# Optimization experiments

Measured on AMD Instinct MI355X. Metric: run time of the kernel, lower is better.

The kernel has to match this reference:

```python
import jax, jax.numpy as jnp
import numpy as np

N_VOX = 1_000_000
GRID = 192
C_IN, C_HID, C_OUT, KVOL = 3, 64, 3, 27
BN_EPS = 1e-5


def _build_neighbor_map(N=N_VOX, grid=GRID, seed=0):
    """Sample N unique voxel coords in a grid^3 volume and build the 27-offset
    kernel map (index of neighbor voxel per offset, -1 if absent), emulating
    MinkowskiEngine's coordinate-manager kernel map for stride-1 3x3x3 conv."""
    rng = np.random.default_rng(seed)
    keys = np.sort(rng.choice(grid ** 3, size=N, replace=False)).astype(np.int64)
    z = keys % grid
    y = (keys // grid) % grid
    x = keys // (grid * grid)
    offs = [(dx, dy, dz) for dx in (-1, 0, 1) for dy in (-1, 0, 1) for dz in (-1, 0, 1)]
    nbr = np.full((KVOL, N), -1, np.int32)
    for k, (dx, dy, dz) in enumerate(offs):
        nx, ny, nz = x + dx, y + dy, z + dz
        inb = (nx >= 0) & (nx < grid) & (ny >= 0) & (ny < grid) & (nz >= 0) & (nz < grid)
        nk = nx * grid * grid + ny * grid + nz
        pos = np.searchsorted(keys, nk).clip(0, N - 1)
        found = inb & (keys[pos] == nk)
        nbr[k] = np.where(found, pos, -1).astype(np.int32)
    return nbr


def setup_inputs() -> dict:
    key = jax.random.key(0)
    k1, k2, k3 = jax.random.split(key, 3)
    nbr = jnp.asarray(_build_neighbor_map())
    feats = jax.random.normal(k1, (N_VOX, C_IN), jnp.float32)
    W1 = jax.random.normal(k2, (KVOL, C_IN, C_HID), jnp.float32) * 0.1
    gamma = jnp.ones((C_HID,), jnp.float32)
    beta = jnp.zeros((C_HID,), jnp.float32)
    W2 = jax.random.normal(k3, (KVOL, C_HID, C_OUT), jnp.float32) * 0.05
    return {"feats": feats, "W1": W1, "gamma": gamma, "beta": beta,
            "W2": W2, "neighbor_idx": nbr}


def reference(feats, W1, gamma, beta, W2, neighbor_idx):
    N = feats.shape[0]
    mask = neighbor_idx >= 0                       # [27, N]
    idx = jnp.where(mask, neighbor_idx, 0)
    # --- sparse conv 3^3, stride 1: gather -> GEMM -> accumulate ---
    g = feats[idx] * mask[..., None]               # [27, N, 3]
    h = jnp.einsum('knc,kcd->nd', g, W1)           # [N, 64]
    # --- BatchNorm (training-mode batch stats) + ReLU ---
    mu = h.mean(0)
    var = h.var(0)
    h = (h - mu) * jax.lax.rsqrt(var + BN_EPS) * gamma + beta
    h = jax.nn.relu(h)
    # --- transposed conv, stride 1: same map with sign-flipped offsets ---
    idx_t = idx[::-1]
    mask_t = mask[::-1]
    def step(acc, kin):
        i, m, w = kin                               # i,m: [N], w: [64,3]
        return acc + jnp.where(m[:, None], h[i], 0.0) @ w, None
    out, _ = jax.lax.scan(step, jnp.zeros((N, C_OUT), feats.dtype),
                          (idx_t, mask_t, W2))
    return out
```

## Files before the change

### kernel.cpp

```cpp
#include <hip/hip_runtime.h>
#include <hip/hip_fp16.h>


#define KVOL 27
#define CHID 64

typedef _Float16 half2_t __attribute__((ext_vector_type(2)));
typedef unsigned int uint32;

static __device__ __forceinline__ float fdot2(uint32 u, uint32 w, float acc) {
    return __builtin_amdgcn_fdot2(__builtin_bit_cast(half2_t, u),
                                  __builtin_bit_cast(half2_t, w), acc, false);
}
static __device__ __forceinline__ uint32 pkh2(float a, float b) {
    auto p = __builtin_amdgcn_cvt_pkrtz(a, b);
    return __builtin_bit_cast(uint32, p);
}
static __device__ __forceinline__ uint32 pk_rne(float a, float b) {
    _Float16 ha = (_Float16)a, hb = (_Float16)b;
    unsigned short ua = __builtin_bit_cast(unsigned short, ha);
    unsigned short ub = __builtin_bit_cast(unsigned short, hb);
    return (uint32)ua | ((uint32)ub << 16);
}
static __device__ __forceinline__ void unpk(uint32 u, float& lo, float& hi) {
    half2_t h = __builtin_bit_cast(half2_t, u);
    lo = (float)h.x; hi = (float)h.y;
}

__global__ __launch_bounds__(256) void k_prep(
    const float* __restrict__ feats, const float* __restrict__ W1,
    const float* __restrict__ W2,
    float* __restrict__ f_t, float* __restrict__ W1t, uint32* __restrict__ w2q,
    uint32* __restrict__ h2, int N, int Ns)
{
    const int b = blockIdx.x;
    if (b == 0) {
        for (int i = threadIdx.x; i < 64 * 81; i += 256) {
            const int d = i / 81, kc = i % 81;
            W1t[i] = W1[kc * 64 + d];
        }
        for (int i = threadIdx.x; i < KVOL * 96; i += 256) {
            const int k = i / 96, r = i % 96;
            const int dc = r / 12, c = (r % 12) / 4, p = r & 3;
            const int d0 = dc * 8 + 2 * p;
            const float* src = W2 + (26 - k) * 192;
            w2q[i] = pk_rne(src[d0 * 3 + c], src[(d0 + 1) * 3 + c]);
        }
        for (int i = threadIdx.x; i < 3 * 64; i += 256) {
            const int c = i >> 6, pp = i & 63;
            f_t[(long long)c * Ns + N + pp] = 0.f;
        }
        for (int i = threadIdx.x; i < 8 * 4; i += 256) {
            const int dc = i >> 2, p = i & 3;
            h2[((long long)dc * Ns + N) * 4 + p] = 0u;
        }
    } else {
        __shared__ float tile[768];
        for (long long t0 = (long long)(b - 1) * 256; t0 < N;
             t0 += (long long)(gridDim.x - 1) * 256) {
            const int nrem = (int)min((long long)256, (long long)N - t0);
            __syncthreads();
            for (int i = threadIdx.x; i < 3 * nrem; i += 256)
                tile[i] = feats[t0 * 3 + i];
            __syncthreads();
            for (int i = threadIdx.x; i < nrem; i += 256) {
                f_t[0 * (long long)Ns + t0 + i] = tile[i * 3 + 0];
                f_t[1 * (long long)Ns + t0 + i] = tile[i * 3 + 1];
                f_t[2 * (long long)Ns + t0 + i] = tile[i * 3 + 2];
            }
        }
    }
}

__global__ __launch_bounds__(256) void k_conv1(
    const float* __restrict__ f_t, const float* __restrict__ W1t,
    const int* __restrict__ nbr, uint32* __restrict__ h2,
    int N, int Ns)
{
    const int lane = threadIdx.x & 63;
    const int tile = (int)((blockIdx.x * 256u + threadIdx.x) >> 6);
    const long long n0 = (long long)tile * 64;
    if (n0 >= N) return;
    const int n = (int)(n0 + lane);

    int j[KVOL];
#pragma unroll
    for (int k = 0; k < KVOL; ++k) j[k] = nbr[(long long)k * N + n];
#pragma unroll
    for (int k = 0; k < KVOL; ++k) j[k] = (j[k] < 0) ? N : j[k];

    float f[3 * KVOL];
#pragma unroll
    for (int k = 0; k < KVOL; ++k) {
        f[3 * k + 0] = f_t[j[k]];
        f[3 * k + 1] = f_t[Ns + j[k]];
        f[3 * k + 2] = f_t[2 * Ns + j[k]];
    }

#pragma unroll 2
    for (int t = 0; t < 32; ++t) {
        const float* __restrict__ w0 = W1t + (2 * t)     * 81;
        const float* __restrict__ w1 = W1t + (2 * t + 1) * 81;
        float a0 = 0.f, a1 = 0.f;
#pragma unroll
        for (int i = 0; i < 81; ++i) {
            a0 = fmaf(f[i], w0[i], a0);
            a1 = fmaf(f[i], w1[i], a1);
        }
        h2[((long long)(t >> 2) * Ns + n) * 4 + (t & 3)] = pkh2(a0, a1);
    }
}

__global__ __launch_bounds__(256) void k_stats(
    const uint32* __restrict__ h2, float* __restrict__ gstats, int N, int Ns)
{
    const int dc = blockIdx.y;
    const uint4* base = (const uint4*)(h2 + (long long)dc * Ns * 4);
    float s[8], q[8];
#pragma unroll
    for (int e = 0; e < 8; ++e) { s[e] = 0.f; q[e] = 0.f; }
    for (long long i = blockIdx.x * 256 + threadIdx.x; i < N;
         i += (long long)gridDim.x * 256) {
        const uint4 u = base[i];
        float lo, hi;
        unpk(u.x, lo, hi); s[0]+=lo; q[0]=fmaf(lo,lo,q[0]); s[1]+=hi; q[1]=fmaf(hi,hi,q[1]);
        unpk(u.y, lo, hi); s[2]+=lo; q[2]=fmaf(lo,lo,q[2]); s[3]+=hi; q[3]=fmaf(hi,hi,q[3]);
        unpk(u.z, lo, hi); s[4]+=lo; q[4]=fmaf(lo,lo,q[4]); s[5]+=hi; q[5]=fmaf(hi,hi,q[5]);
        unpk(u.w, lo, hi); s[6]+=lo; q[6]=fmaf(lo,lo,q[6]); s[7]+=hi; q[7]=fmaf(hi,hi,q[7]);
    }
#pragma unroll
    for (int e = 0; e < 8; ++e)
        for (int off = 32; off > 0; off >>= 1) {
            s[e] += __shfl_down(s[e], off);
            q[e] += __shfl_down(q[e], off);
        }
    __shared__ float red[4][16];
    const int wib = threadIdx.x >> 6, lane = threadIdx.x & 63;
    if (lane == 0) {
#pragma unroll
        for (int e = 0; e < 8; ++e) { red[wib][e] = s[e]; red[wib][8 + e] = q[e]; }
    }
    __syncthreads();
    if (threadIdx.x < 16) {
        const float v = red[0][threadIdx.x] + red[1][threadIdx.x]
                      + red[2][threadIdx.x] + red[3][threadIdx.x];
        const int e = threadIdx.x & 7;
        const int d = dc * 8 + e;
        atomicAdd(&gstats[threadIdx.x < 8 ? d : 64 + d], v);
    }
}

__global__ void k_bn(const float* __restrict__ gstats,
                     const float* __restrict__ gamma,
                     const float* __restrict__ beta,
                     float* __restrict__ sc_sh, float invN)
{
    const int d = threadIdx.x;
    const float mu  = gstats[d] * invN;
    const float var = gstats[64 + d] * invN - mu * mu;
    const float sc  = gamma[d] * rsqrtf(var + 1e-5f);
    sc_sh[d]      = sc;
    sc_sh[64 + d] = beta[d] - mu * sc;
}

__global__ __launch_bounds__(256) void k_apply(
    uint32* __restrict__ h2, const float* __restrict__ sc_sh, int N, int Ns)
{
    const int dc = blockIdx.y;
    float sc[8], sh[8];
#pragma unroll
    for (int e = 0; e < 8; ++e) {
        sc[e] = sc_sh[dc * 8 + e];
        sh[e] = sc_sh[64 + dc * 8 + e];
    }
    uint4* base = (uint4*)(h2 + (long long)dc * Ns * 4);
    for (long long i = blockIdx.x * 256 + threadIdx.x; i < N;
         i += (long long)gridDim.x * 256) {
        uint4 u = base[i];
        float lo, hi; uint4 r;
        unpk(u.x, lo, hi);
        r.x = pkh2(fmaxf(fmaf(lo, sc[0], sh[0]), 0.f), fmaxf(fmaf(hi, sc[1], sh[1]), 0.f));
        unpk(u.y, lo, hi);
        r.y = pkh2(fmaxf(fmaf(lo, sc[2], sh[2]), 0.f), fmaxf(fmaf(hi, sc[3], sh[3]), 0.f));
        unpk(u.z, lo, hi);
        r.z = pkh2(fmaxf(fmaf(lo, sc[4], sh[4]), 0.f), fmaxf(fmaf(hi, sc[5], sh[5]), 0.f));
        unpk(u.w, lo, hi);
        r.w = pkh2(fmaxf(fmaf(lo, sc[6], sh[6]), 0.f), fmaxf(fmaf(hi, sc[7], sh[7]), 0.f));
        base[i] = r;
    }
}

__global__ __launch_bounds__(256) void k_conv2(
    const uint32* __restrict__ h2, const uint32* __restrict__ w2q,
    const int* __restrict__ nbr, float* __restrict__ out,
    int N, int Ns, int nblk)
{
    const int bid = blockIdx.x;
    const int qq = nblk >> 3, rr = nblk & 7;
    const int xcd = bid & 7, pos = bid >> 3;
    const int sb = (xcd < rr) ? xcd * (qq + 1) + pos
                              : rr * (qq + 1) + (xcd - rr) * qq + pos;
    const int lane = threadIdx.x & 63;
    const int tile = sb * 4 + (threadIdx.x >> 6);
    const long long n0 = (long long)tile * 64;
    if (n0 >= N) return;
    const int n = (int)(n0 + lane);

    float a0 = 0.f, a1 = 0.f, a2 = 0.f;
    int jn = nbr[n];
    for (int k = 0; k < KVOL; ++k) {
        const int j = (jn < 0) ? N : jn;
        if (k + 1 < KVOL) jn = nbr[(long long)(k + 1) * N + n];

        uint4 u[8];
#pragma unroll
        for (int dc = 0; dc < 8; ++dc)
            u[dc] = *(const uint4*)(h2 + ((long long)dc * Ns + j) * 4);

        const uint32* __restrict__ w = w2q + k * 96;
#pragma unroll
        for (int dc = 0; dc < 8; ++dc) {
            const int wb = dc * 12;
            a0 = fdot2(u[dc].x, w[wb + 0], a0);
            a1 = fdot2(u[dc].x, w[wb + 4], a1);
            a2 = fdot2(u[dc].x, w[wb + 8], a2);
            a0 = fdot2(u[dc].y, w[wb + 1], a0);
            a1 = fdot2(u[dc].y, w[wb + 5], a1);
            a2 = fdot2(u[dc].y, w[wb + 9], a2);
            a0 = fdot2(u[dc].z, w[wb + 2], a0);
            a1 = fdot2(u[dc].z, w[wb + 6], a1);
            a2 = fdot2(u[dc].z, w[wb + 10], a2);
            a0 = fdot2(u[dc].w, w[wb + 3], a0);
            a1 = fdot2(u[dc].w, w[wb + 7], a1);
            a2 = fdot2(u[dc].w, w[wb + 11], a2);
        }
    }
    out[3LL * n + 0] = a0;
    out[3LL * n + 1] = a1;
    out[3LL * n + 2] = a2;
}

extern "C" void kernel_launch(void* const* d_in, const int* in_sizes, int n_in,
                              void* d_out, int out_size, void* d_ws, size_t ws_size,
                              hipStream_t stream) {
    const float* feats = (const float*)d_in[0];
    const float* W1    = (const float*)d_in[1];
    const float* gamma = (const float*)d_in[2];
    const float* beta  = (const float*)d_in[3];
    const float* W2    = (const float*)d_in[4];
    const int*   nbr   = (const int*)  d_in[5];
    const int N  = in_sizes[0] / 3;
    const int Ns = N + 64;
    float* out = (float*)d_out;

    char* ws = (char*)d_ws;
    uint32* h2 = (uint32*)ws;
    size_t off = (size_t)8 * Ns * 16;
    float* f_t = (float*)(ws + off);
    off += (size_t)3 * Ns * sizeof(float);
    float* W1t = (float*)(ws + off);
    off += (size_t)64 * 81 * sizeof(float);
    uint32* w2q = (uint32*)(ws + off);
    off += (size_t)KVOL * 96 * sizeof(uint32);
    float* gstats = (float*)(ws + off);
    float* sc_sh  = gstats + 128;

    (void)hipMemsetAsync(gstats, 0, 128 * sizeof(float), stream);

    const int ntiles = (N + 63) / 64;
    const int nblk   = (ntiles + 3) / 4;

    k_prep <<<257, 256, 0, stream>>>(feats, W1, W2, f_t, W1t, w2q, h2, N, Ns);
    k_conv1<<<nblk, 256, 0, stream>>>(f_t, W1t, nbr, h2, N, Ns);
    k_stats<<<dim3(256, 8), 256, 0, stream>>>(h2, gstats, N, Ns);
    k_bn   <<<1, 64, 0, stream>>>(gstats, gamma, beta, sc_sh, 1.0f / (float)N);
    k_apply<<<dim3(256, 8), 256, 0, stream>>>(h2, sc_sh, N, Ns);
    k_conv2<<<nblk, 256, 0, stream>>>(h2, w2q, nbr, out, N, Ns, nblk);
}
```

Before: 582.4 us.

## Compact valid neighbor pairs for conv2, fuse BN-ReLU into gather, fp16 conv1

A new pass compacts the valid (output, neighbor) pairs for each of the 27 offsets into a list. The second conv then walks only those pairs and accumulates into the output with atomics, so it no longer gathers h rows for absent neighbors. The BN scale and shift are applied as packed fp16 plus ReLU inside the conv2 gather, which removes the separate apply pass over h. Conv1 now packs features and weights to fp16 and uses dot2 instructions, and it counts valid neighbors per offset with ballots. In exchange there is an extra read of the neighbor map, pair-list writes, float atomics on the output with a memset, and more fp16 rounding.

```diff
diff --git a/kernel.cpp b/kernel.cpp
--- a/kernel.cpp
+++ b/kernel.cpp
@@ -7,6 +7,7 @@
 
 typedef _Float16 half2_t __attribute__((ext_vector_type(2)));
 typedef unsigned int uint32;
+typedef unsigned long long u64;
 
 static __device__ __forceinline__ float fdot2(uint32 u, uint32 w, float acc) {
     return __builtin_amdgcn_fdot2(__builtin_bit_cast(half2_t, u),
@@ -26,18 +27,37 @@
     half2_t h = __builtin_bit_cast(half2_t, u);
     lo = (float)h.x; hi = (float)h.y;
 }
+static __device__ __forceinline__ uint32 bnrelu(uint32 h, uint32 sc, uint32 sh) {
+    half2_t r = __builtin_bit_cast(half2_t, h) * __builtin_bit_cast(half2_t, sc)
+              + __builtin_bit_cast(half2_t, sh);
+    uint32 u = __builtin_bit_cast(uint32, r);
+    uint32 s = (u & 0x80008000u) >> 15;
+    return u & ~(s * 0xFFFFu);
+}
+
+#define M_GSTATS 0
+#define M_CNT8   128
+#define M_STARTS 344
+#define M_ENDS   372
+#define M_CURSOR 399
+#define M_SCPK   426
+#define M_SHPK   458
+#define M_WORDS  490
 
 __global__ __launch_bounds__(256) void k_prep(
     const float* __restrict__ feats, const float* __restrict__ W1,
     const float* __restrict__ W2,
-    float* __restrict__ f_t, float* __restrict__ W1t, uint32* __restrict__ w2q,
+    float* __restrict__ f_t, uint32* __restrict__ w1q, uint32* __restrict__ w2q,
     uint32* __restrict__ h2, int N, int Ns)
 {
     const int b = blockIdx.x;
     if (b == 0) {
-        for (int i = threadIdx.x; i < 64 * 81; i += 256) {
-            const int d = i / 81, kc = i % 81;
-            W1t[i] = W1[kc * 64 + d];
+        for (int i = threadIdx.x; i < 64 * 41; i += 256) {
+            const int d = i / 41, p = i % 41;
+            const int kc0 = 2 * p, kc1 = 2 * p + 1;
+            const float v0 = W1[kc0 * 64 + d];
+            const float v1 = (kc1 < 81) ? W1[kc1 * 64 + d] : 0.f;
+            w1q[i] = pk_rne(v0, v1);
         }
         for (int i = threadIdx.x; i < KVOL * 96; i += 256) {
             const int k = i / 96, r = i % 96;
@@ -72,43 +92,58 @@
     }
 }
 
-__global__ __launch_bounds__(256) void k_conv1(
-    const float* __restrict__ f_t, const float* __restrict__ W1t,
+__global__ __launch_bounds__(256, 4) void k_conv1(
+    const float* __restrict__ f_t, const uint32* __restrict__ w1q,
     const int* __restrict__ nbr, uint32* __restrict__ h2,
-    int N, int Ns)
-{
+    uint32* __restrict__ cnt8, int N, int Ns)
+{
+    __shared__ uint32 lcnt[KVOL];
+    if (threadIdx.x < KVOL) lcnt[threadIdx.x] = 0;
+    __syncthreads();
+
     const int lane = threadIdx.x & 63;
     const int tile = (int)((blockIdx.x * 256u + threadIdx.x) >> 6);
     const long long n0 = (long long)tile * 64;
-    if (n0 >= N) return;
-    const int n = (int)(n0 + lane);
-
-    int j[KVOL];
-#pragma unroll
-    for (int k = 0; k < KVOL; ++k) j[k] = nbr[(long long)k * N + n];
-#pragma unroll
-    for (int k = 0; k < KVOL; ++k) j[k] = (j[k] < 0) ? N : j[k];
-
-    float f[3 * KVOL];
-#pragma unroll
-    for (int k = 0; k < KVOL; ++k) {
-        f[3 * k + 0] = f_t[j[k]];
-        f[3 * k + 1] = f_t[Ns + j[k]];
-        f[3 * k + 2] = f_t[2 * Ns + j[k]];
-    }
+    const bool active = (n0 < N);
+
+    if (active) {
+        const int n = (int)(n0 + lane);
+        int j[KVOL];
+#pragma unroll
+        for (int k = 0; k < KVOL; ++k) {
+            const int jr = nbr[(long long)k * N + n];
+            const u64 m = __ballot(jr >= 0);
+            if (lane == 0) atomicAdd(&lcnt[k], (uint32)__popcll(m));
+            j[k] = (jr < 0) ? N : jr;
+        }
+
+        uint32 fh[41];
+#pragma unroll
+        for (int p = 0; p < 41; ++p) {
+            const int kc0 = 2 * p, kc1 = 2 * p + 1;
+            const float x0 = f_t[(long long)(kc0 % 3) * Ns + j[kc0 / 3]];
+            const float x1 = (kc1 < 81)
+                ? f_t[(long long)(kc1 % 3) * Ns + j[kc1 / 3]] : 0.f;
+            fh[p] = pkh2(x0, x1);
+        }
 
 #pragma unroll 2
-    for (int t = 0; t < 32; ++t) {
-        const float* __restrict__ w0 = W1t + (2 * t)     * 81;
-        const float* __restrict__ w1 = W1t + (2 * t + 1) * 81;
-        float a0 = 0.f, a1 = 0.f;
-#pragma unroll
-        for (int i = 0; i < 81; ++i) {
-            a0 = fmaf(f[i], w0[i], a0);
-            a1 = fmaf(f[i], w1[i], a1);
-        }
-        h2[((long long)(t >> 2) * Ns + n) * 4 + (t & 3)] = pkh2(a0, a1);
-    }
+        for (int t = 0; t < 32; ++t) {
+            const uint32* __restrict__ w0 = w1q + (2 * t) * 41;
+            const uint32* __restrict__ w1 = w1q + (2 * t + 1) * 41;
+            float a0 = 0.f, a1 = 0.f;
+#pragma unroll
+            for (int p = 0; p < 41; ++p) {
+                a0 = fdot2(fh[p], w0[p], a0);
+                a1 = fdot2(fh[p], w1[p], a1);
+            }
+            h2[((long long)(t >> 2) * Ns + n) * 4 + (t & 3)] = pkh2(a0, a1);
+        }
+    }
+
+    __syncthreads();
+    if (threadIdx.x < KVOL)
+        atomicAdd(&cnt8[(blockIdx.x & 7) * KVOL + threadIdx.x], lcnt[threadIdx.x]);
 }
 
 __global__ __launch_bounds__(256) void k_stats(
@@ -150,67 +185,114 @@
     }
 }
 
-__global__ void k_bn(const float* __restrict__ gstats,
-                     const float* __restrict__ gamma,
-                     const float* __restrict__ beta,
-                     float* __restrict__ sc_sh, float invN)
-{
-    const int d = threadIdx.x;
-    const float mu  = gstats[d] * invN;
-    const float var = gstats[64 + d] * invN - mu * mu;
-    const float sc  = gamma[d] * rsqrtf(var + 1e-5f);
-    sc_sh[d]      = sc;
-    sc_sh[64 + d] = beta[d] - mu * sc;
-}
-
-__global__ __launch_bounds__(256) void k_apply(
-    uint32* __restrict__ h2, const float* __restrict__ sc_sh, int N, int Ns)
-{
-    const int dc = blockIdx.y;
-    float sc[8], sh[8];
-#pragma unroll
-    for (int e = 0; e < 8; ++e) {
-        sc[e] = sc_sh[dc * 8 + e];
-        sh[e] = sc_sh[64 + dc * 8 + e];
-    }
-    uint4* base = (uint4*)(h2 + (long long)dc * Ns * 4);
-    for (long long i = blockIdx.x * 256 + threadIdx.x; i < N;
-         i += (long long)gridDim.x * 256) {
-        uint4 u = base[i];
-        float lo, hi; uint4 r;
-        unpk(u.x, lo, hi);
-        r.x = pkh2(fmaxf(fmaf(lo, sc[0], sh[0]), 0.f), fmaxf(fmaf(hi, sc[1], sh[1]), 0.f));
-        unpk(u.y, lo, hi);
-        r.y = pkh2(fmaxf(fmaf(lo, sc[2], sh[2]), 0.f), fmaxf(fmaf(hi, sc[3], sh[3]), 0.f));
-        unpk(u.z, lo, hi);
-        r.z = pkh2(fmaxf(fmaf(lo, sc[4], sh[4]), 0.f), fmaxf(fmaf(hi, sc[5], sh[5]), 0.f));
-        unpk(u.w, lo, hi);
-        r.w = pkh2(fmaxf(fmaf(lo, sc[6], sh[6]), 0.f), fmaxf(fmaf(hi, sc[7], sh[7]), 0.f));
-        base[i] = r;
+__global__ void k_scan(uint32* __restrict__ meta,
+                       const float* __restrict__ gamma,
+                       const float* __restrict__ beta, float invN)
+{
+    __shared__ float scv[64], shv[64];
+    __shared__ uint32 scnt[KVOL];
+    const int t = threadIdx.x;
+    if (t < KVOL) {
+        uint32 c = 0;
+        for (int r = 0; r < 8; ++r) c += meta[M_CNT8 + r * KVOL + t];
+        scnt[t] = c;
+    }
+    {
+        const float* gstats = (const float*)meta;
+        const float mu  = gstats[t] * invN;
+        const float var = gstats[64 + t] * invN - mu * mu;
+        const float sc  = gamma[t] * rsqrtf(var + 1e-5f);
+        scv[t] = sc;
+        shv[t] = beta[t] - mu * sc;
+    }
+    __syncthreads();
+    if (t == 0) {
+        uint32 s = 0;
+        for (int k = 0; k < KVOL; ++k) {
+            meta[M_STARTS + k] = s;
+            meta[M_CURSOR + k] = s;
+            meta[M_ENDS + k]   = s + scnt[k];
+            s += (scnt[k] + 63u) & ~63u;
+        }
+        meta[M_STARTS + KVOL] = s;
+    }
+    if (t < 32) {
+        meta[M_SCPK + t] = pk_rne(scv[2 * t], scv[2 * t + 1]);
+        meta[M_SHPK + t] = pk_rne(shv[2 * t], shv[2 * t + 1]);
+    }
+}
+
+__global__ __launch_bounds__(256) void k_fill(
+    const int* __restrict__ nbr, uint32* __restrict__ meta,
+    int2* __restrict__ pairs, int N, uint32 cap)
+{
+    __shared__ int lbuf[2048];
+    __shared__ uint32 wcnt[4];
+    __shared__ uint32 sbase, srun;
+    const int k = blockIdx.y;
+    const int nb = blockIdx.x * 2048;
+    const int tid = threadIdx.x;
+    const int wib = tid >> 6, lane = tid & 63;
+
+    uint32 mycnt = 0;
+#pragma unroll
+    for (int r = 0; r < 8; ++r) {
+        const int i = nb + r * 256 + tid;
+        const int v = (i < N) ? nbr[(long long)k * N + i] : -1;
+        lbuf[r * 256 + tid] = v;
+        mycnt += (v >= 0);
+    }
+    for (int off = 32; off > 0; off >>= 1) mycnt += __shfl_down(mycnt, off);
+    if (lane == 0) wcnt[wib] = mycnt;
+    __syncthreads();
+    if (tid == 0) {
+        const uint32 C = wcnt[0] + wcnt[1] + wcnt[2] + wcnt[3];
+        sbase = atomicAdd(&meta[M_CURSOR + k], C);
+        srun = 0;
+    }
+    __syncthreads();
+    const uint32 base = sbase;
+
+    for (int r = 0; r < 8; ++r) {
+        const int i = r * 256 + tid;
+        const int jv = lbuf[i];
+        const bool v = (jv >= 0);
+        const u64 m = __ballot(v);
+        if (lane == 0) wcnt[wib] = (uint32)__popcll(m);
+        __syncthreads();
+        uint32 woff = srun;
+        for (int w = 0; w < 4; ++w) if (w < wib) woff += wcnt[w];
+        const uint32 pos = woff + (uint32)__popcll(m & ((1ull << lane) - 1ull));
+        if (v && base + pos < cap)
+            pairs[base + pos] = make_int2(nb + i, jv);
+        __syncthreads();
+        if (tid == 0) srun += wcnt[0] + wcnt[1] + wcnt[2] + wcnt[3];
+        __syncthreads();
     }
 }
 
 __global__ __launch_bounds__(256) void k_conv2(
     const uint32* __restrict__ h2, const uint32* __restrict__ w2q,
-    const int* __restrict__ nbr, float* __restrict__ out,
-    int N, int Ns, int nblk)
-{
-    const int bid = blockIdx.x;
-    const int qq = nblk >> 3, rr = nblk & 7;
-    const int xcd = bid & 7, pos = bid >> 3;
-    const int sb = (xcd < rr) ? xcd * (qq + 1) + pos
-                              : rr * (qq + 1) + (xcd - rr) * qq + pos;
+    const uint32* __restrict__ meta, const int2* __restrict__ pairs,
+    float* __restrict__ out, int N, int Ns)
+{
     const int lane = threadIdx.x & 63;
-    const int tile = sb * 4 + (threadIdx.x >> 6);
-    const long long n0 = (long long)tile * 64;
-    if (n0 >= N) return;
-    const int n = (int)(n0 + lane);
-
-    float a0 = 0.f, a1 = 0.f, a2 = 0.f;
-    int jn = nbr[n];
-    for (int k = 0; k < KVOL; ++k) {
-        const int j = (jn < 0) ? N : jn;
-        if (k + 1 < KVOL) jn = nbr[(long long)(k + 1) * N + n];
+    const int wid = (blockIdx.x << 2) + (threadIdx.x >> 6);
+    const int nwv = gridDim.x << 2;
+    const uint32 P = meta[M_STARTS + KVOL];
+
+    uint32 scl[32], shl[32];
+#pragma unroll
+    for (int i = 0; i < 32; ++i) { scl[i] = meta[M_SCPK + i]; shl[i] = meta[M_SHPK + i]; }
+
+    for (uint32 base = (uint32)wid * 64u; base < P; base += (uint32)nwv * 64u) {
+        int k = 0;
+        while (k < KVOL - 1 && base >= meta[M_STARTS + k + 1]) ++k;
+        const uint32 send = meta[M_ENDS + k];
+        const uint32 idx = base + lane;
+        const bool act = idx < send;
+        int n = 0, j = N;
+        if (act) { const int2 pr = pairs[idx]; n = pr.x; j = pr.y; }
 
         uint4 u[8];
 #pragma unroll
@@ -218,26 +300,33 @@
             u[dc] = *(const uint4*)(h2 + ((long long)dc * Ns + j) * 4);
 
         const uint32* __restrict__ w = w2q + k * 96;
+        float a0 = 0.f, a1 = 0.f, a2 = 0.f;
 #pragma unroll
         for (int dc = 0; dc < 8; ++dc) {
-            const int wb = dc * 12;
-            a0 = fdot2(u[dc].x, w[wb + 0], a0);
-            a1 = fdot2(u[dc].x, w[wb + 4], a1);
-            a2 = fdot2(u[dc].x, w[wb + 8], a2);
-            a0 = fdot2(u[dc].y, w[wb + 1], a0);
-            a1 = fdot2(u[dc].y, w[wb + 5], a1);
-            a2 = fdot2(u[dc].y, w[wb + 9], a2);
-            a0 = fdot2(u[dc].z, w[wb + 2], a0);
-            a1 = fdot2(u[dc].z, w[wb + 6], a1);
-            a2 = fdot2(u[dc].z, w[wb + 10], a2);
-            a0 = fdot2(u[dc].w, w[wb + 3], a0);
-            a1 = fdot2(u[dc].w, w[wb + 7], a1);
-            a2 = fdot2(u[dc].w, w[wb + 11], a2);
-        }
-    }
-    out[3LL * n + 0] = a0;
-    out[3LL * n + 1] = a1;
-    out[3LL * n + 2] = a2;
+            const int wb = dc * 12, sb = dc * 4;
+            const uint32 h0 = bnrelu(u[dc].x, scl[sb + 0], shl[sb + 0]);
+            const uint32 h1 = bnrelu(u[dc].y, scl[sb + 1], shl[sb + 1]);
+            const uint32 h2w = bnrelu(u[dc].z, scl[sb + 2], shl[sb + 2]);
+            const uint32 h3 = bnrelu(u[dc].w, scl[sb + 3], shl[sb + 3]);
+            a0 = fdot2(h0, w[wb + 0], a0);
+            a1 = fdot2(h0, w[wb + 4], a1);
+            a2 = fdot2(h0, w[wb + 8], a2);
+            a0 = fdot2(h1, w[wb + 1], a0);
+            a1 = fdot2(h1, w[wb + 5], a1);
+            a2 = fdot2(h1, w[wb + 9], a2);
+            a0 = fdot2(h2w, w[wb + 2], a0);
+            a1 = fdot2(h2w, w[wb + 6], a1);
+            a2 = fdot2(h2w, w[wb + 10], a2);
+            a0 = fdot2(h3, w[wb + 3], a0);
+            a1 = fdot2(h3, w[wb + 7], a1);
+            a2 = fdot2(h3, w[wb + 11], a2);
+        }
+        if (act) {
+            atomicAdd(&out[3LL * n + 0], a0);
+            atomicAdd(&out[3LL * n + 1], a1);
+            atomicAdd(&out[3LL * n + 2], a2);
+        }
+    }
 }
 
 extern "C" void kernel_launch(void* const* d_in, const int* in_sizes, int n_in,
@@ -256,24 +345,21 @@
     char* ws = (char*)d_ws;
     uint32* h2 = (uint32*)ws;
     size_t off = (size_t)8 * Ns * 16;
-    float* f_t = (float*)(ws + off);
-    off += (size_t)3 * Ns * sizeof(float);
-    float* W1t = (float*)(ws + off);
-    off += (size_t)64 * 81 * sizeof(float);
-    uint32* w2q = (uint32*)(ws + off);
-    off += (size_t)KVOL * 96 * sizeof(uint32);
-    float* gstats = (float*)(ws + off);
-    float* sc_sh  = gstats + 128;
-
-    (void)hipMemsetAsync(gstats, 0, 128 * sizeof(float), stream);
-
-    const int ntiles = (N + 63) / 64;
-    const int nblk   = (ntiles + 3) / 4;
-
-    k_prep <<<257, 256, 0, stream>>>(feats, W1, W2, f_t, W1t, w2q, h2, N, Ns);
-    k_conv1<<<nblk, 256, 0, stream>>>(f_t, W1t, nbr, h2, N, Ns);
-    k_stats<<<dim3(256, 8), 256, 0, stream>>>(h2, gstats, N, Ns);
-    k_bn   <<<1, 64, 0, stream>>>(gstats, gamma, beta, sc_sh, 1.0f / (float)N);
-    k_apply<<<dim3(256, 8), 256, 0, stream>>>(h2, sc_sh, N, Ns);
-    k_conv2<<<nblk, 256, 0, stream>>>(h2, w2q, nbr, out, N, Ns, nblk);
-}
+    uint32* w2q = (uint32*)(ws + off); off += KVOL * 96 * 4;
+    uint32* meta = (uint32*)(ws + off); off += ((M_WORDS * 4 + 255) & ~255ull);
+    float*  f_t = (float*)(ws + off);
+    uint32* w1q = (uint32*)(ws + off + (size_t)3 * Ns * 4);
+    int2*   pairs = (int2*)(ws + off);
+    const uint32 cap = (uint32)((ws_size - off) / sizeof(int2));
+
+    (void)hipMemsetAsync(meta, 0, (M_CNT8 + 8 * KVOL) * 4, stream);
+    (void)hipMemsetAsync(out, 0, (size_t)out_size * 4, stream);
+
+    const int nblk = (N / 64 + 3) / 4;
+    k_prep <<<257, 256, 0, stream>>>(feats, W1, W2, f_t, w1q, w2q, h2, N, Ns);
+    k_conv1<<<nblk, 256, 0, stream>>>(f_t, w1q, nbr, h2, (uint32*)(meta + M_CNT8), N, Ns);
+    k_stats<<<dim3(256, 8), 256, 0, stream>>>(h2, (float*)meta, N, Ns);
+    k_scan <<<1, 64, 0, stream>>>(meta, gamma, beta, 1.0f / (float)N);
+    k_fill <<<dim3((N + 2047) / 2048, KVOL), 256, 0, stream>>>(nbr, meta, pairs, N, cap);
+    k_conv2<<<2048, 256, 0, stream>>>(h2, w2q, meta, pairs, out, N, Ns);
+}
```

Result: slower. 1.011 ms (+73.6%).

## Store hidden activations row-major per voxel and use fp16 dot2 in conv1

Applied to the files above, without the earlier changes.

The hidden fp16 tensor moves from eight channel-group planes to one contiguous 128-byte row per voxel. Each neighbour gather in conv2 now reads a single cache-line-sized row instead of eight 16-byte pieces spread across separate planes. Conv1 now packs gathered features and W1 into half2 and accumulates with fdot2, which halves the arithmetic instruction count at some cost in precision. Stats and apply are adapted to the interleaved layout, and occupancy hints are added to both conv kernels. The block count now assumes N is a multiple of 64.

```diff
diff --git a/kernel.cpp b/kernel.cpp
--- a/kernel.cpp
+++ b/kernel.cpp
@@ -3,7 +3,6 @@
 
 
 #define KVOL 27
-#define CHID 64
 
 typedef _Float16 half2_t __attribute__((ext_vector_type(2)));
 typedef unsigned int uint32;
@@ -30,19 +29,22 @@
 __global__ __launch_bounds__(256) void k_prep(
     const float* __restrict__ feats, const float* __restrict__ W1,
     const float* __restrict__ W2,
-    float* __restrict__ f_t, float* __restrict__ W1t, uint32* __restrict__ w2q,
-    uint32* __restrict__ h2, int N, int Ns)
+    float* __restrict__ f_t, uint32* __restrict__ w1q, uint32* __restrict__ w2q,
+    uint32* __restrict__ h32, int N, int Ns)
 {
     const int b = blockIdx.x;
     if (b == 0) {
-        for (int i = threadIdx.x; i < 64 * 81; i += 256) {
-            const int d = i / 81, kc = i % 81;
-            W1t[i] = W1[kc * 64 + d];
+        for (int i = threadIdx.x; i < 64 * 41; i += 256) {
+            const int d = i / 41, p = i % 41;
+            const int kc0 = 2 * p, kc1 = 2 * p + 1;
+            const float v0 = W1[kc0 * 64 + d];
+            const float v1 = (kc1 < 81) ? W1[kc1 * 64 + d] : 0.f;
+            w1q[i] = pk_rne(v0, v1);
         }
         for (int i = threadIdx.x; i < KVOL * 96; i += 256) {
             const int k = i / 96, r = i % 96;
-            const int dc = r / 12, c = (r % 12) / 4, p = r & 3;
-            const int d0 = dc * 8 + 2 * p;
+            const int g = r / 12, c = (r % 12) / 4, p = r & 3;
+            const int d0 = g * 8 + 2 * p;
             const float* src = W2 + (26 - k) * 192;
             w2q[i] = pk_rne(src[d0 * 3 + c], src[(d0 + 1) * 3 + c]);
         }
@@ -50,10 +52,8 @@
             const int c = i >> 6, pp = i & 63;
             f_t[(long long)c * Ns + N + pp] = 0.f;
         }
-        for (int i = threadIdx.x; i < 8 * 4; i += 256) {
-            const int dc = i >> 2, p = i & 3;
-            h2[((long long)dc * Ns + N) * 4 + p] = 0u;
-        }
+        if (threadIdx.x < 32)
+            h32[(long long)N * 32 + threadIdx.x] = 0u;
     } else {
         __shared__ float tile[768];
         for (long long t0 = (long long)(b - 1) * 256; t0 < N;
@@ -72,9 +72,9 @@
     }
 }
 
-__global__ __launch_bounds__(256) void k_conv1(
-    const float* __restrict__ f_t, const float* __restrict__ W1t,
-    const int* __restrict__ nbr, uint32* __restrict__ h2,
+__global__ __launch_bounds__(256, 4) void k_conv1(
+    const float* __restrict__ f_t, const uint32* __restrict__ w1q,
+    const int* __restrict__ nbr, uint32* __restrict__ h32,
     int N, int Ns)
 {
     const int lane = threadIdx.x & 63;
@@ -89,39 +89,48 @@
 #pragma unroll
     for (int k = 0; k < KVOL; ++k) j[k] = (j[k] < 0) ? N : j[k];
 
-    float f[3 * KVOL];
-#pragma unroll
-    for (int k = 0; k < KVOL; ++k) {
-        f[3 * k + 0] = f_t[j[k]];
-        f[3 * k + 1] = f_t[Ns + j[k]];
-        f[3 * k + 2] = f_t[2 * Ns + j[k]];
-    }
-
-#pragma unroll 2
-    for (int t = 0; t < 32; ++t) {
-        const float* __restrict__ w0 = W1t + (2 * t)     * 81;
-        const float* __restrict__ w1 = W1t + (2 * t + 1) * 81;
-        float a0 = 0.f, a1 = 0.f;
-#pragma unroll
-        for (int i = 0; i < 81; ++i) {
-            a0 = fmaf(f[i], w0[i], a0);
-            a1 = fmaf(f[i], w1[i], a1);
-        }
-        h2[((long long)(t >> 2) * Ns + n) * 4 + (t & 3)] = pkh2(a0, a1);
+    uint32 fh[41];
+#pragma unroll
+    for (int p = 0; p < 41; ++p) {
+        const int kc0 = 2 * p, kc1 = 2 * p + 1;
+        const float x0 = f_t[(long long)(kc0 % 3) * Ns + j[kc0 / 3]];
+        const float x1 = (kc1 < 81)
+            ? f_t[(long long)(kc1 % 3) * Ns + j[kc1 / 3]] : 0.f;
+        fh[p] = pkh2(x0, x1);
+    }
+
+    uint32* __restrict__ hrow = h32 + (long long)n * 32;
+#pragma unroll
+    for (int g = 0; g < 8; ++g) {
+        uint32 wd[4];
+#pragma unroll
+        for (int p4 = 0; p4 < 4; ++p4) {
+            const int t = 4 * g + p4;
+            const uint32* __restrict__ w0 = w1q + (2 * t) * 41;
+            const uint32* __restrict__ w1 = w1q + (2 * t + 1) * 41;
+            float a0 = 0.f, a1 = 0.f;
+#pragma unroll
+            for (int p = 0; p < 41; ++p) {
+                a0 = fdot2(fh[p], w0[p], a0);
+                a1 = fdot2(fh[p], w1[p], a1);
+            }
+            wd[p4] = pkh2(a0, a1);
+        }
+        *(uint4*)(hrow + 4 * g) = make_uint4(wd[0], wd[1], wd[2], wd[3]);
     }
 }
 
 __global__ __launch_bounds__(256) void k_stats(
-    const uint32* __restrict__ h2, float* __restrict__ gstats, int N, int Ns)
-{
-    const int dc = blockIdx.y;
-    const uint4* base = (const uint4*)(h2 + (long long)dc * Ns * 4);
+    const uint4* __restrict__ h4, float* __restrict__ gstats, int N)
+{
+    const int tid = threadIdx.x;
+    const int g = tid & 7;
     float s[8], q[8];
 #pragma unroll
     for (int e = 0; e < 8; ++e) { s[e] = 0.f; q[e] = 0.f; }
-    for (long long i = blockIdx.x * 256 + threadIdx.x; i < N;
-         i += (long long)gridDim.x * 256) {
-        const uint4 u = base[i];
+    const int total = N * 8;
+    for (int i = blockIdx.x * 256 + tid; i < total; i += gridDim.x * 256) {
+        const uint4 u = h4[i];
         float lo, hi;
         unpk(u.x, lo, hi); s[0]+=lo; q[0]=fmaf(lo,lo,q[0]); s[1]+=hi; q[1]=fmaf(hi,hi,q[1]);
         unpk(u.y, lo, hi); s[2]+=lo; q[2]=fmaf(lo,lo,q[2]); s[3]+=hi; q[3]=fmaf(hi,hi,q[3]);
@@ -129,24 +138,27 @@
         unpk(u.w, lo, hi); s[6]+=lo; q[6]=fmaf(lo,lo,q[6]); s[7]+=hi; q[7]=fmaf(hi,hi,q[7]);
     }
 #pragma unroll
-    for (int e = 0; e < 8; ++e)
-        for (int off = 32; off > 0; off >>= 1) {
-            s[e] += __shfl_down(s[e], off);
-            q[e] += __shfl_down(q[e], off);
-        }
-    __shared__ float red[4][16];
-    const int wib = threadIdx.x >> 6, lane = threadIdx.x & 63;
-    if (lane == 0) {
-#pragma unroll
-        for (int e = 0; e < 8; ++e) { red[wib][e] = s[e]; red[wib][8 + e] = q[e]; }
+    for (int e = 0; e < 8; ++e) {
+        for (int m = 8; m < 64; m <<= 1) {
+            s[e] += __shfl_xor(s[e], m);
+            q[e] += __shfl_xor(q[e], m);
+        }
+    }
+    __shared__ float sred[4][8][8], qred[4][8][8];
+    const int wib = tid >> 6, lane = tid & 63;
+    if (lane < 8) {
+#pragma unroll
+        for (int e = 0; e < 8; ++e) { sred[wib][lane][e] = s[e]; qred[wib][lane][e] = q[e]; }
     }
     __syncthreads();
-    if (threadIdx.x < 16) {
-        const float v = red[0][threadIdx.x] + red[1][threadIdx.x]
-                      + red[2][threadIdx.x] + red[3][threadIdx.x];
-        const int e = threadIdx.x & 7;
-        const int d = dc * 8 + e;
-        atomicAdd(&gstats[threadIdx.x < 8 ? d : 64 + d], v);
+    if (tid < 64) {
+        const int gg = tid >> 3, e = tid & 7;
+        atomicAdd(&gstats[tid], sred[0][gg][e] + sred[1][gg][e]
+                              + sred[2][gg][e] + sred[3][gg][e]);
+    } else if (tid < 128) {
+        const int d = tid - 64, gg = d >> 3, e = d & 7;
+        atomicAdd(&gstats[64 + d], qred[0][gg][e] + qred[1][gg][e]
+                                 + qred[2][gg][e] + qred[3][gg][e]);
     }
 }
 
@@ -164,19 +176,19 @@
 }
 
 __global__ __launch_bounds__(256) void k_apply(
-    uint32* __restrict__ h2, const float* __restrict__ sc_sh, int N, int Ns)
-{
-    const int dc = blockIdx.y;
+    uint4* __restrict__ h4, const float* __restrict__ sc_sh, int N)
+{
+    const int tid = threadIdx.x;
+    const int g = tid & 7;
     float sc[8], sh[8];
 #pragma unroll
     for (int e = 0; e < 8; ++e) {
-        sc[e] = sc_sh[dc * 8 + e];
-        sh[e] = sc_sh[64 + dc * 8 + e];
-    }
-    uint4* base = (uint4*)(h2 + (long long)dc * Ns * 4);
-    for (long long i = blockIdx.x * 256 + threadIdx.x; i < N;
-         i += (long long)gridDim.x * 256) {
-        uint4 u = base[i];
+        sc[e] = sc_sh[8 * g + e];
+        sh[e] = sc_sh[64 + 8 * g + e];
+    }
+    const int total = N * 8;
+    for (int i = blockIdx.x * 256 + tid; i < total; i += gridDim.x * 256) {
+        uint4 u = h4[i];
         float lo, hi; uint4 r;
         unpk(u.x, lo, hi);
         r.x = pkh2(fmaxf(fmaf(lo, sc[0], sh[0]), 0.f), fmaxf(fmaf(hi, sc[1], sh[1]), 0.f));
@@ -186,14 +198,14 @@
         r.z = pkh2(fmaxf(fmaf(lo, sc[4], sh[4]), 0.f), fmaxf(fmaf(hi, sc[5], sh[5]), 0.f));
         unpk(u.w, lo, hi);
         r.w = pkh2(fmaxf(fmaf(lo, sc[6], sh[6]), 0.f), fmaxf(fmaf(hi, sc[7], sh[7]), 0.f));
-        base[i] = r;
-    }
-}
-
-__global__ __launch_bounds__(256) void k_conv2(
-    const uint32* __restrict__ h2, const uint32* __restrict__ w2q,
+        h4[i] = r;
+    }
+}
+
+__global__ __launch_bounds__(256, 6) void k_conv2(
+    const uint4* __restrict__ h4, const uint32* __restrict__ w2q,
     const int* __restrict__ nbr, float* __restrict__ out,
-    int N, int Ns, int nblk)
+    int N, int nblk)
 {
     const int bid = blockIdx.x;
     const int qq = nblk >> 3, rr = nblk & 7;
@@ -212,27 +224,27 @@
         const int j = (jn < 0) ? N : jn;
         if (k + 1 < KVOL) jn = nbr[(long long)(k + 1) * N + n];
 
+        const uint4* __restrict__ row = h4 + (long long)j * 8;
         uint4 u[8];
 #pragma unroll
-        for (int dc = 0; dc < 8; ++dc)
-            u[dc] = *(const uint4*)(h2 + ((long long)dc * Ns + j) * 4);
+        for (int g = 0; g < 8; ++g) u[g] = row[g];
 
         const uint32* __restrict__ w = w2q + k * 96;
 #pragma unroll
-        for (int dc = 0; dc < 8; ++dc) {
-            const int wb = dc * 12;
-            a0 = fdot2(u[dc].x, w[wb + 0], a0);
-            a1 = fdot2(u[dc].x, w[wb + 4], a1);
-            a2 = fdot2(u[dc].x, w[wb + 8], a2);
-            a0 = fdot2(u[dc].y, w[wb + 1], a0);
-            a1 = fdot2(u[dc].y, w[wb + 5], a1);
-            a2 = fdot2(u[dc].y, w[wb + 9], a2);
-            a0 = fdot2(u[dc].z, w[wb + 2], a0);
-            a1 = fdot2(u[dc].z, w[wb + 6], a1);
-            a2 = fdot2(u[dc].z, w[wb + 10], a2);
-            a0 = fdot2(u[dc].w, w[wb + 3], a0);
-            a1 = fdot2(u[dc].w, w[wb + 7], a1);
-            a2 = fdot2(u[dc].w, w[wb + 11], a2);
+        for (int g = 0; g < 8; ++g) {
+            const int wb = g * 12;
+            a0 = fdot2(u[g].x, w[wb + 0], a0);
+            a1 = fdot2(u[g].x, w[wb + 4], a1);
+            a2 = fdot2(u[g].x, w[wb + 8], a2);
+            a0 = fdot2(u[g].y, w[wb + 1], a0);
+            a1 = fdot2(u[g].y, w[wb + 5], a1);
+            a2 = fdot2(u[g].y, w[wb + 9], a2);
+            a0 = fdot2(u[g].z, w[wb + 2], a0);
+            a1 = fdot2(u[g].z, w[wb + 6], a1);
+            a2 = fdot2(u[g].z, w[wb + 10], a2);
+            a0 = fdot2(u[g].w, w[wb + 3], a0);
+            a1 = fdot2(u[g].w, w[wb + 7], a1);
+            a2 = fdot2(u[g].w, w[wb + 11], a2);
         }
     }
     out[3LL * n + 0] = a0;
@@ -254,26 +266,22 @@
     float* out = (float*)d_out;
 
     char* ws = (char*)d_ws;
-    uint32* h2 = (uint32*)ws;
-    size_t off = (size_t)8 * Ns * 16;
-    float* f_t = (float*)(ws + off);
-    off += (size_t)3 * Ns * sizeof(float);
-    float* W1t = (float*)(ws + off);
-    off += (size_t)64 * 81 * sizeof(float);
-    uint32* w2q = (uint32*)(ws + off);
-    off += (size_t)KVOL * 96 * sizeof(uint32);
+    uint32* h32 = (uint32*)ws;
+    size_t off = (((size_t)(N + 1) * 128) + 255) & ~(size_t)255;
+    float* f_t = (float*)(ws + off); off += (size_t)3 * Ns * 4;
+    uint32* w1q = (uint32*)(ws + off); off += (size_t)64 * 41 * 4;
+    uint32* w2q = (uint32*)(ws + off); off += (size_t)KVOL * 96 * 4;
     float* gstats = (float*)(ws + off);
     float* sc_sh  = gstats + 128;
 
     (void)hipMemsetAsync(gstats, 0, 128 * sizeof(float), stream);
 
-    const int ntiles = (N + 63) / 64;
-    const int nblk   = (ntiles + 3) / 4;
-
-    k_prep <<<257, 256, 0, stream>>>(feats, W1, W2, f_t, W1t, w2q, h2, N, Ns);
-    k_conv1<<<nblk, 256, 0, stream>>>(f_t, W1t, nbr, h2, N, Ns);
-    k_stats<<<dim3(256, 8), 256, 0, stream>>>(h2, gstats, N, Ns);
+    const int nblk = (N / 64 + 3) / 4;
+
+    k_prep <<<257, 256, 0, stream>>>(feats, W1, W2, f_t, w1q, w2q, h32, N, Ns);
+    k_conv1<<<nblk, 256, 0, stream>>>(f_t, w1q, nbr, h32, N, Ns);
+    k_stats<<<2048, 256, 0, stream>>>((const uint4*)h32, gstats, N);
     k_bn   <<<1, 64, 0, stream>>>(gstats, gamma, beta, sc_sh, 1.0f / (float)N);
-    k_apply<<<dim3(256, 8), 256, 0, stream>>>(h2, sc_sh, N, Ns);
-    k_conv2<<<nblk, 256, 0, stream>>>(h2, w2q, nbr, out, N, Ns, nblk);
-}
+    k_apply<<<2048, 256, 0, stream>>>((uint4*)h32, sc_sh, N);
+    k_conv2<<<nblk, 256, 0, stream>>>((const uint4*)h32, w2q, nbr, out, N, nblk);
+}
```

Measured after the change: 578.7 us. Within noise of the previous version (-0.6%).
